# Kernel optimization log

Hardware: AMD Instinct MI355X
Metric: run time of the kernel (lower is better)

Reference implementation:

```python
import jax, jax.numpy as jnp
import numpy as np

INPUT_DIM = 1024
OUTPUT_DIM = 512
N_QUBITS = 12
DEPTH = 8
BATCH = 32768
LN_EPS = 1e-5
NOISE = 0.01


def setup_inputs() -> dict:
    key = jax.random.key(0)
    ks = jax.random.split(key, 12)
    inp = {
        "x": jax.random.normal(ks[0], (BATCH, INPUT_DIM), dtype=jnp.float32),
        "w_in": jax.random.normal(ks[1], (N_QUBITS, INPUT_DIM), dtype=jnp.float32) * 0.03,
        "b_in": jnp.zeros((N_QUBITS,), jnp.float32),
        "ln_g": jnp.ones((N_QUBITS,), jnp.float32),
        "ln_b": jnp.zeros((N_QUBITS,), jnp.float32),
        "rot": jax.random.normal(ks[2], (DEPTH, N_QUBITS, 3), dtype=jnp.float32) * 0.1,
        "ent": jax.random.normal(ks[3], (DEPTH, N_QUBITS - 1), dtype=jnp.float32) * 0.1,
        "w1": jax.random.normal(ks[4], (N_QUBITS, N_QUBITS), dtype=jnp.float32) * 0.3,
        "b1": jnp.zeros((N_QUBITS,), jnp.float32),
        "w2": jax.random.normal(ks[5], (OUTPUT_DIM, N_QUBITS), dtype=jnp.float32) * 0.3,
        "b2": jnp.zeros((OUTPUT_DIM,), jnp.float32),
        "meas_basis": jax.random.normal(ks[6], (N_QUBITS,), dtype=jnp.float32) * 0.1,
    }
    return inp


def _entangle(state, c):
    # c: sigmoid(ent[layer]) shape [n-1]. Effective (traced) torch semantics:
    # out[i]   = s[i]*(1-c_i)   + s[i+1]*c_i     for i in 0..n-2
    # out[n-1] = s[n-1]*(1-c_{n-2}) + s[n-2]*c_{n-2}
    left = state[:, :-1] * (1.0 - c) + state[:, 1:] * c          # [B, n-1]
    last = state[:, -1] * (1.0 - c[-1]) + state[:, -2] * c[-1]   # [B]
    return jnp.concatenate([left, last[:, None]], axis=1)


def reference(x, w_in, b_in, ln_g, ln_b, rot, ent, w1, b1, w2, b2, meas_basis):
    # input layer + layernorm + tanh
    h = x @ w_in.T + b_in                                   # [B, n]
    mu = jnp.mean(h, axis=-1, keepdims=True)
    var = jnp.mean((h - mu) ** 2, axis=-1, keepdims=True)
    h = (h - mu) * jax.lax.rsqrt(var + LN_EPS) * ln_g + ln_b
    h = jnp.tanh(h)

    encoded = h * jnp.float32(np.pi)
    state = jnp.zeros_like(encoded)
    for layer in range(DEPTH):
        rx = encoded + rot[layer, :, 0]
        state = state * jnp.cos(rx * 0.5) + jnp.sin(rot[layer, :, 1] * 0.5)
        state = state * jnp.cos(rot[layer, :, 2] * 0.5)     # Re(exp(i*rz/2))
        if layer < DEPTH - 1:
            state = _entangle(state, jax.nn.sigmoid(ent[layer]))

    # measurement: basis rotation + gaussian noise + tanh
    measured = state * jnp.tanh(meas_basis)
    noise = jax.random.normal(jax.random.key(1234), measured.shape, dtype=measured.dtype) * NOISE
    measured = jnp.tanh(measured + noise)

    # output MLP
    out = jax.nn.relu(measured @ w1.T + b1) @ w2.T + b2     # [B, OUTPUT_DIM]
    return out
```

## Files before the change

kernel.cpp:

```cpp
#include <hip/hip_runtime.h>
#include <cstdint>
#include <cstddef>


__device__ __forceinline__ uint32_t rotl32(uint32_t x, int r) {
  return (x << r) | (x >> (32 - r));
}

__device__ __forceinline__ void threefry2x32(uint32_t k0, uint32_t k1,
                                             uint32_t& x0, uint32_t& x1) {
  const uint32_t k2 = k0 ^ k1 ^ 0x1BD11BDAu;
  x0 += k0; x1 += k1;
#define TF_R(r) { x0 += x1; x1 = rotl32(x1, (r)); x1 ^= x0; }
  TF_R(13) TF_R(15) TF_R(26) TF_R(6)
  x0 += k1; x1 += k2 + 1u;
  TF_R(17) TF_R(29) TF_R(16) TF_R(24)
  x0 += k2; x1 += k0 + 2u;
  TF_R(13) TF_R(15) TF_R(26) TF_R(6)
  x0 += k0; x1 += k1 + 3u;
  TF_R(17) TF_R(29) TF_R(16) TF_R(24)
  x0 += k1; x1 += k2 + 4u;
  TF_R(13) TF_R(15) TF_R(26) TF_R(6)
  x0 += k2; x1 += k0 + 5u;
#undef TF_R
}

__device__ __forceinline__ float erfinv_xla(float x) {
  float w = -log1pf(-x * x);
  float p;
  if (w < 5.0f) {
    w -= 2.5f;
    p = 2.81022636e-08f;
    p = fmaf(p, w, 3.43273939e-07f);
    p = fmaf(p, w, -3.5233877e-06f);
    p = fmaf(p, w, -4.39150654e-06f);
    p = fmaf(p, w, 0.00021858087f);
    p = fmaf(p, w, -0.00125372503f);
    p = fmaf(p, w, -0.00417768164f);
    p = fmaf(p, w, 0.246640727f);
    p = fmaf(p, w, 1.50140941f);
  } else {
    w = sqrtf(w) - 3.0f;
    p = -0.000200214257f;
    p = fmaf(p, w, 0.000100950558f);
    p = fmaf(p, w, 0.00134934322f);
    p = fmaf(p, w, -0.00367342844f);
    p = fmaf(p, w, 0.00573950773f);
    p = fmaf(p, w, -0.0076224613f);
    p = fmaf(p, w, 0.00943887047f);
    p = fmaf(p, w, 1.00167406f);
    p = fmaf(p, w, 2.83297682f);
  }
  return p * x;
}

__global__ __launch_bounds__(512, 4)
void qnn_gemm_in(const float* __restrict__ x, const float* __restrict__ w_in,
                 const float* __restrict__ b_in, float* __restrict__ h) {
  __shared__ float wl[12 * 1024];
  {
    const float4* ws = (const float4*)w_in;
    float4* wd = (float4*)wl;
#pragma unroll
    for (int j = 0; j < 6; ++j) wd[threadIdx.x + 512 * j] = ws[threadIdx.x + 512 * j];
  }
  __syncthreads();

  const int wave = threadIdx.x >> 6;
  const int lane = threadIdx.x & 63;
  const int r    = lane >> 4;
  const int kc   = lane & 15;

  float bq[12];
#pragma unroll
  for (int q = 0; q < 12; ++q) bq[q] = b_in[q];

#pragma unroll
  for (int it = 0; it < 2; ++it) {
    const int row = (blockIdx.x << 6) + (wave << 3) + (it << 2) + r;
    const float4* xr = (const float4*)(x + (size_t)row * 1024);

    float4 A[4], B[4];
#pragma unroll
    for (int i = 0; i < 4; ++i) A[i] = xr[((0 + i) << 4) + kc];
#pragma unroll
    for (int i = 0; i < 4; ++i) B[i] = xr[((4 + i) << 4) + kc];

    float acc[12];
#pragma unroll
    for (int q = 0; q < 12; ++q) acc[q] = 0.0f;

#pragma unroll
    for (int i = 0; i < 4; ++i) {
      const int ks = i;
#pragma unroll
      for (int q = 0; q < 12; ++q) {
        const float4 wv = *(const float4*)&wl[q * 1024 + (ks << 6) + (kc << 2)];
        acc[q] += A[i].x * wv.x + A[i].y * wv.y + A[i].z * wv.z + A[i].w * wv.w;
      }
    }
#pragma unroll
    for (int i = 0; i < 4; ++i) A[i] = xr[((8 + i) << 4) + kc];

#pragma unroll
    for (int i = 0; i < 4; ++i) {
      const int ks = 4 + i;
#pragma unroll
      for (int q = 0; q < 12; ++q) {
        const float4 wv = *(const float4*)&wl[q * 1024 + (ks << 6) + (kc << 2)];
        acc[q] += B[i].x * wv.x + B[i].y * wv.y + B[i].z * wv.z + B[i].w * wv.w;
      }
    }
#pragma unroll
    for (int i = 0; i < 4; ++i) B[i] = xr[((12 + i) << 4) + kc];

#pragma unroll
    for (int i = 0; i < 4; ++i) {
      const int ks = 8 + i;
#pragma unroll
      for (int q = 0; q < 12; ++q) {
        const float4 wv = *(const float4*)&wl[q * 1024 + (ks << 6) + (kc << 2)];
        acc[q] += A[i].x * wv.x + A[i].y * wv.y + A[i].z * wv.z + A[i].w * wv.w;
      }
    }
#pragma unroll
    for (int i = 0; i < 4; ++i) {
      const int ks = 12 + i;
#pragma unroll
      for (int q = 0; q < 12; ++q) {
        const float4 wv = *(const float4*)&wl[q * 1024 + (ks << 6) + (kc << 2)];
        acc[q] += B[i].x * wv.x + B[i].y * wv.y + B[i].z * wv.z + B[i].w * wv.w;
      }
    }

#pragma unroll
    for (int q = 0; q < 12; ++q) {
      float v = acc[q];
      v += __shfl_xor(v, 1);
      v += __shfl_xor(v, 2);
      v += __shfl_xor(v, 4);
      v += __shfl_xor(v, 8);
      acc[q] = v + bq[q];
    }
    if (kc == 0) {
      float* hp = h + (size_t)row * 12;
      *(float4*)(hp + 0) = make_float4(acc[0], acc[1], acc[2], acc[3]);
      *(float4*)(hp + 4) = make_float4(acc[4], acc[5], acc[6], acc[7]);
      *(float4*)(hp + 8) = make_float4(acc[8], acc[9], acc[10], acc[11]);
    }
  }
}

__global__ __launch_bounds__(256, 4)
void qnn_tail(const float* __restrict__ h_in,
              const float* __restrict__ ln_g, const float* __restrict__ ln_b,
              const float* __restrict__ rot,  const float* __restrict__ ent,
              const float* __restrict__ w1,   const float* __restrict__ b1,
              const float* __restrict__ w2,   const float* __restrict__ b2,
              const float* __restrict__ meas, float* __restrict__ out) {
  __shared__ float w2s[512 * 12];
  __shared__ float b2s[512];
  __shared__ float hid[32 * 12];
  __shared__ float rot0s[8 * 16], sr1s[8 * 16], cr2s[8 * 16], cens[8 * 16];
  __shared__ float tmbs[16], w1T[12 * 16], b1s[16], lgs[16], lbs[16];

  const int t = threadIdx.x;

  {
    const float4* s = (const float4*)w2;
    float4* d = (float4*)w2s;
#pragma unroll
    for (int j = 0; j < 6; ++j) d[t + 256 * j] = s[t + 256 * j];
    if (t < 128) ((float4*)b2s)[t] = ((const float4*)b2)[t];
    if (t < 96) {
      const int l = t / 12, q = t % 12, base = (l * 12 + q) * 3;
      rot0s[l * 16 + q] = rot[base + 0];
      sr1s[l * 16 + q]  = sinf(rot[base + 1] * 0.5f);
      cr2s[l * 16 + q]  = cosf(rot[base + 2] * 0.5f);
    }
    if (t >= 96 && t < 184) {
      const int i = t - 96, l = i / 11, q = i % 11;
      cens[l * 16 + q] = 1.0f / (1.0f + expf(-ent[l * 11 + q]));
    }
    if (t >= 184 && t < 196) tmbs[t - 184] = tanhf(meas[t - 184]);
    if (t >= 196 && t < 208) b1s[t - 196] = b1[t - 196];
    if (t >= 208 && t < 220) lgs[t - 208] = ln_g[t - 208];
    if (t >= 220 && t < 232) lbs[t - 220] = ln_b[t - 220];
    if (t < 144) { const int j = t / 12, q = t % 12; w1T[q * 16 + j] = w1[t]; }
  }
  __syncthreads();

  float wa[12], wb[12];
#pragma unroll
  for (int q = 0; q < 12; ++q) {
    wa[q] = w2s[t * 12 + q];
    wb[q] = w2s[(t + 256) * 12 + q];
  }
  const float ba = b2s[t], bb = b2s[t + 256];

  const int lane = t & 63;
  const int wv   = t >> 6;
  const int grp  = lane >> 4;
  const int q    = lane & 15;
  const int gb   = lane & 48;
  const bool act = (q < 12);
  const int cidx = (q == 11) ? 10 : q;

#pragma unroll
  for (int pass = 0; pass < 2; ++pass) {
    const int rl  = (pass << 4) + (wv << 2) + grp;
    const int row = (blockIdx.x << 5) + rl;

    float hq = act ? h_in[(size_t)row * 12 + q] : 0.0f;

    float s = hq;
    s += __shfl_xor(s, 1); s += __shfl_xor(s, 2);
    s += __shfl_xor(s, 4); s += __shfl_xor(s, 8);
    const float mu = s * (1.0f / 12.0f);
    float d = act ? (hq - mu) : 0.0f;
    float v2 = d * d;
    v2 += __shfl_xor(v2, 1); v2 += __shfl_xor(v2, 2);
    v2 += __shfl_xor(v2, 4); v2 += __shfl_xor(v2, 8);
    const float inv = 1.0f / sqrtf(v2 * (1.0f / 12.0f) + 1e-5f);

    const float n   = d * inv * lgs[q] + lbs[q];
    const float enc = tanhf(n) * 3.14159265358979f;

    float st = 0.0f;
#pragma unroll
    for (int l = 0; l < 8; ++l) {
      const float rx = enc + rot0s[l * 16 + q];
      st = st * cosf(rx * 0.5f) + sr1s[l * 16 + q];
      st *= cr2s[l * 16 + q];
      if (l < 7) {
        const float stn = __shfl(st, lane + 1);
        const float stp = __shfl(st, lane - 1);
        const float c   = cens[l * 16 + cidx];
        const float other = (q == 11) ? stp : stn;
        st = st * (1.0f - c) + other * c;
      }
    }

    uint32_t x0 = 0u, x1 = (uint32_t)row * 12u + (uint32_t)q;
    threefry2x32(0u, 1234u, x0, x1);
    const uint32_t bits = x0 ^ x1;
    const float u01 = __uint_as_float((bits >> 9) | 0x3F800000u) - 1.0f;
    float u = u01 * 2.0f + (-0.99999994f);
    u = fmaxf(-0.99999994f, u);
    const float nrm = 1.41421356237f * erfinv_xla(u);
    const float m = tanhf(st * tmbs[q] + nrm * 0.01f);

    float acc1 = b1s[q];
#pragma unroll
    for (int qq = 0; qq < 12; ++qq) {
      const float mq = __shfl(m, gb + qq);
      acc1 = fmaf(mq, w1T[qq * 16 + q], acc1);
    }
    if (act) hid[rl * 12 + q] = fmaxf(acc1, 0.0f);
  }
  __syncthreads();

  float* ob = out + (size_t)blockIdx.x * 32 * 512;
  for (int rr = 0; rr < 32; ++rr) {
    const float4 h0 = *(const float4*)&hid[rr * 12 + 0];
    const float4 h1 = *(const float4*)&hid[rr * 12 + 4];
    const float4 h2 = *(const float4*)&hid[rr * 12 + 8];
    const float hvv[12] = {h0.x, h0.y, h0.z, h0.w, h1.x, h1.y, h1.z, h1.w,
                           h2.x, h2.y, h2.z, h2.w};
    float a = ba, b = bb;
#pragma unroll
    for (int qq = 0; qq < 12; ++qq) {
      a = fmaf(hvv[qq], wa[qq], a);
      b = fmaf(hvv[qq], wb[qq], b);
    }
    ob[rr * 512 + t] = a;
    ob[rr * 512 + 256 + t] = b;
  }
}

extern "C" void kernel_launch(void* const* d_in, const int* in_sizes, int n_in,
                              void* d_out, int out_size, void* d_ws, size_t ws_size,
                              hipStream_t stream) {
  const float* x    = (const float*)d_in[0];
  const float* w_in = (const float*)d_in[1];
  const float* b_in = (const float*)d_in[2];
  const float* ln_g = (const float*)d_in[3];
  const float* ln_b = (const float*)d_in[4];
  const float* rot  = (const float*)d_in[5];
  const float* ent  = (const float*)d_in[6];
  const float* w1   = (const float*)d_in[7];
  const float* b1   = (const float*)d_in[8];
  const float* w2   = (const float*)d_in[9];
  const float* b2   = (const float*)d_in[10];
  const float* mb   = (const float*)d_in[11];
  float* outp = (float*)d_out;
  float* h    = (float*)d_ws;

  qnn_gemm_in<<<512, 512, 0, stream>>>(x, w_in, b_in, h);
  qnn_tail<<<1024, 256, 0, stream>>>(h, ln_g, ln_b, rot, ent, w1, b1, w2, b2, mb, outp);
}
```

Baseline: 250.0 us.

## Restructure input GEMM so each wave processes four rows with shared weight loads

The input projection kernel now gives each wave four rows at once, with every lane covering a strided slice of K. Each LDS weight float4 is reused across four rows instead of one, and accumulation uses fused multiply-adds. Blocks shrink to 256 threads and the grid doubles to 1024. The trade-offs are a full 64-lane shuffle reduction per output, a larger register footprint (48 accumulators plus 16 float4 inputs), and a more serialized global load pattern per wave.

```diff
diff --git a/kernel.cpp b/kernel.cpp
--- a/kernel.cpp
+++ b/kernel.cpp
@@ -54,7 +54,7 @@
   return p * x;
 }
 
-__global__ __launch_bounds__(512, 4)
+__global__ __launch_bounds__(256, 2)
 void qnn_gemm_in(const float* __restrict__ x, const float* __restrict__ w_in,
                  const float* __restrict__ b_in, float* __restrict__ h) {
   __shared__ float wl[12 * 1024];
@@ -62,91 +62,65 @@
     const float4* ws = (const float4*)w_in;
     float4* wd = (float4*)wl;
 #pragma unroll
-    for (int j = 0; j < 6; ++j) wd[threadIdx.x + 512 * j] = ws[threadIdx.x + 512 * j];
+    for (int j = 0; j < 12; ++j) wd[threadIdx.x + 256 * j] = ws[threadIdx.x + 256 * j];
   }
   __syncthreads();
 
   const int wave = threadIdx.x >> 6;
   const int lane = threadIdx.x & 63;
-  const int r    = lane >> 4;
-  const int kc   = lane & 15;
-
-  float bq[12];
-#pragma unroll
-  for (int q = 0; q < 12; ++q) bq[q] = b_in[q];
-
-#pragma unroll
-  for (int it = 0; it < 2; ++it) {
-    const int row = (blockIdx.x << 6) + (wave << 3) + (it << 2) + r;
-    const float4* xr = (const float4*)(x + (size_t)row * 1024);
-
-    float4 A[4], B[4];
-#pragma unroll
-    for (int i = 0; i < 4; ++i) A[i] = xr[((0 + i) << 4) + kc];
-#pragma unroll
-    for (int i = 0; i < 4; ++i) B[i] = xr[((4 + i) << 4) + kc];
-
-    float acc[12];
-#pragma unroll
-    for (int q = 0; q < 12; ++q) acc[q] = 0.0f;
-
-#pragma unroll
-    for (int i = 0; i < 4; ++i) {
-      const int ks = i;
+  const float bmy = (lane < 12) ? b_in[lane] : 0.0f;
+
+#pragma unroll
+  for (int blk = 0; blk < 2; ++blk) {
+    const int row0 = (blockIdx.x << 5) + (wave << 3) + (blk << 2);
+
+    float4 xv[4][4];
+#pragma unroll
+    for (int r = 0; r < 4; ++r) {
+      const float4* xr = (const float4*)(x + (size_t)(row0 + r) * 1024);
+#pragma unroll
+      for (int ks = 0; ks < 4; ++ks) xv[r][ks] = xr[(ks << 6) + lane];
+    }
+
+    float acc[4][12];
+#pragma unroll
+    for (int r = 0; r < 4; ++r)
+#pragma unroll
+      for (int q = 0; q < 12; ++q) acc[r][q] = 0.0f;
+
+#pragma unroll
+    for (int q = 0; q < 12; ++q) {
+#pragma unroll
+      for (int ks = 0; ks < 4; ++ks) {
+        const float4 wv = *(const float4*)&wl[q * 1024 + (ks << 8) + (lane << 2)];
+#pragma unroll
+        for (int r = 0; r < 4; ++r) {
+          acc[r][q] = fmaf(xv[r][ks].x, wv.x,
+                      fmaf(xv[r][ks].y, wv.y,
+                      fmaf(xv[r][ks].z, wv.z,
+                      fmaf(xv[r][ks].w, wv.w, acc[r][q]))));
+        }
+      }
+    }
+
+#pragma unroll
+    for (int r = 0; r < 4; ++r) {
+      float hv[12];
 #pragma unroll
       for (int q = 0; q < 12; ++q) {
-        const float4 wv = *(const float4*)&wl[q * 1024 + (ks << 6) + (kc << 2)];
-        acc[q] += A[i].x * wv.x + A[i].y * wv.y + A[i].z * wv.z + A[i].w * wv.w;
+        float v = acc[r][q];
+        v += __shfl_xor(v, 1);
+        v += __shfl_xor(v, 2);
+        v += __shfl_xor(v, 4);
+        v += __shfl_xor(v, 8);
+        v += __shfl_xor(v, 16);
+        v += __shfl_xor(v, 32);
+        hv[q] = v;
       }
-    }
-#pragma unroll
-    for (int i = 0; i < 4; ++i) A[i] = xr[((8 + i) << 4) + kc];
-
-#pragma unroll
-    for (int i = 0; i < 4; ++i) {
-      const int ks = 4 + i;
-#pragma unroll
-      for (int q = 0; q < 12; ++q) {
-        const float4 wv = *(const float4*)&wl[q * 1024 + (ks << 6) + (kc << 2)];
-        acc[q] += B[i].x * wv.x + B[i].y * wv.y + B[i].z * wv.z + B[i].w * wv.w;
-      }
-    }
-#pragma unroll
-    for (int i = 0; i < 4; ++i) B[i] = xr[((12 + i) << 4) + kc];
-
-#pragma unroll
-    for (int i = 0; i < 4; ++i) {
-      const int ks = 8 + i;
-#pragma unroll
-      for (int q = 0; q < 12; ++q) {
-        const float4 wv = *(const float4*)&wl[q * 1024 + (ks << 6) + (kc << 2)];
-        acc[q] += A[i].x * wv.x + A[i].y * wv.y + A[i].z * wv.z + A[i].w * wv.w;
-      }
-    }
-#pragma unroll
-    for (int i = 0; i < 4; ++i) {
-      const int ks = 12 + i;
-#pragma unroll
-      for (int q = 0; q < 12; ++q) {
-        const float4 wv = *(const float4*)&wl[q * 1024 + (ks << 6) + (kc << 2)];
-        acc[q] += B[i].x * wv.x + B[i].y * wv.y + B[i].z * wv.z + B[i].w * wv.w;
-      }
-    }
-
-#pragma unroll
-    for (int q = 0; q < 12; ++q) {
-      float v = acc[q];
-      v += __shfl_xor(v, 1);
-      v += __shfl_xor(v, 2);
-      v += __shfl_xor(v, 4);
-      v += __shfl_xor(v, 8);
-      acc[q] = v + bq[q];
-    }
-    if (kc == 0) {
-      float* hp = h + (size_t)row * 12;
-      *(float4*)(hp + 0) = make_float4(acc[0], acc[1], acc[2], acc[3]);
-      *(float4*)(hp + 4) = make_float4(acc[4], acc[5], acc[6], acc[7]);
-      *(float4*)(hp + 8) = make_float4(acc[8], acc[9], acc[10], acc[11]);
+      float outv = hv[0];
+#pragma unroll
+      for (int q = 1; q < 12; ++q) outv = (lane == q) ? hv[q] : outv;
+      if (lane < 12) h[(size_t)(row0 + r) * 12 + lane] = outv + bmy;
     }
   }
 }
@@ -296,6 +270,6 @@
   float* outp = (float*)d_out;
   float* h    = (float*)d_ws;
 
-  qnn_gemm_in<<<512, 512, 0, stream>>>(x, w_in, b_in, h);
+  qnn_gemm_in<<<1024, 256, 0, stream>>>(x, w_in, b_in, h);
   qnn_tail<<<1024, 256, 0, stream>>>(h, ln_g, ln_b, rot, ent, w1, b1, w2, b2, mb, outp);
 }
```

New measurement: 272.5 us. 9.0% more time.

## Read input-projection weights directly from global memory and shrink GEMM blocks

Applied to the files above, without the earlier changes.

Stops staging the 48KB w_in matrix in shared memory and reads weight float4s straight from global memory, relying on L1/L2 caching. Blocks shrink to 256 threads handling 16 rows each, with a 2048-block grid instead of 512 blocks of 64 rows. This removes the per-block LDS fill and barrier, and lowers LDS use so more blocks can be resident. In exchange, every block fetches the weights again through cache, and the manual double-buffered prefetch of x is replaced by a plain unrolled loop.

```diff
diff --git a/kernel.cpp b/kernel.cpp
--- a/kernel.cpp
+++ b/kernel.cpp
@@ -54,100 +54,49 @@
   return p * x;
 }
 
-__global__ __launch_bounds__(512, 4)
+__global__ __launch_bounds__(256, 4)
 void qnn_gemm_in(const float* __restrict__ x, const float* __restrict__ w_in,
                  const float* __restrict__ b_in, float* __restrict__ h) {
-  __shared__ float wl[12 * 1024];
-  {
-    const float4* ws = (const float4*)w_in;
-    float4* wd = (float4*)wl;
-#pragma unroll
-    for (int j = 0; j < 6; ++j) wd[threadIdx.x + 512 * j] = ws[threadIdx.x + 512 * j];
-  }
-  __syncthreads();
-
   const int wave = threadIdx.x >> 6;
   const int lane = threadIdx.x & 63;
   const int r    = lane >> 4;
   const int kc   = lane & 15;
 
+  const int row = (blockIdx.x << 4) + (wave << 2) + r;
+  const float4* xr = (const float4*)(x + (size_t)row * 1024);
+
   float bq[12];
 #pragma unroll
   for (int q = 0; q < 12; ++q) bq[q] = b_in[q];
 
-#pragma unroll
-  for (int it = 0; it < 2; ++it) {
-    const int row = (blockIdx.x << 6) + (wave << 3) + (it << 2) + r;
-    const float4* xr = (const float4*)(x + (size_t)row * 1024);
-
-    float4 A[4], B[4];
-#pragma unroll
-    for (int i = 0; i < 4; ++i) A[i] = xr[((0 + i) << 4) + kc];
-#pragma unroll
-    for (int i = 0; i < 4; ++i) B[i] = xr[((4 + i) << 4) + kc];
-
-    float acc[12];
-#pragma unroll
-    for (int q = 0; q < 12; ++q) acc[q] = 0.0f;
-
-#pragma unroll
-    for (int i = 0; i < 4; ++i) {
-      const int ks = i;
-#pragma unroll
-      for (int q = 0; q < 12; ++q) {
-        const float4 wv = *(const float4*)&wl[q * 1024 + (ks << 6) + (kc << 2)];
-        acc[q] += A[i].x * wv.x + A[i].y * wv.y + A[i].z * wv.z + A[i].w * wv.w;
-      }
-    }
-#pragma unroll
-    for (int i = 0; i < 4; ++i) A[i] = xr[((8 + i) << 4) + kc];
-
-#pragma unroll
-    for (int i = 0; i < 4; ++i) {
-      const int ks = 4 + i;
-#pragma unroll
-      for (int q = 0; q < 12; ++q) {
-        const float4 wv = *(const float4*)&wl[q * 1024 + (ks << 6) + (kc << 2)];
-        acc[q] += B[i].x * wv.x + B[i].y * wv.y + B[i].z * wv.z + B[i].w * wv.w;
-      }
-    }
-#pragma unroll
-    for (int i = 0; i < 4; ++i) B[i] = xr[((12 + i) << 4) + kc];
-
-#pragma unroll
-    for (int i = 0; i < 4; ++i) {
-      const int ks = 8 + i;
-#pragma unroll
-      for (int q = 0; q < 12; ++q) {
-        const float4 wv = *(const float4*)&wl[q * 1024 + (ks << 6) + (kc << 2)];
-        acc[q] += A[i].x * wv.x + A[i].y * wv.y + A[i].z * wv.z + A[i].w * wv.w;
-      }
-    }
-#pragma unroll
-    for (int i = 0; i < 4; ++i) {
-      const int ks = 12 + i;
-#pragma unroll
-      for (int q = 0; q < 12; ++q) {
-        const float4 wv = *(const float4*)&wl[q * 1024 + (ks << 6) + (kc << 2)];
-        acc[q] += B[i].x * wv.x + B[i].y * wv.y + B[i].z * wv.z + B[i].w * wv.w;
-      }
-    }
-
+  float acc[12];
+#pragma unroll
+  for (int q = 0; q < 12; ++q) acc[q] = 0.0f;
+
+#pragma unroll 4
+  for (int ks = 0; ks < 16; ++ks) {
+    const float4 xv = xr[(ks << 4) + kc];
 #pragma unroll
     for (int q = 0; q < 12; ++q) {
-      float v = acc[q];
-      v += __shfl_xor(v, 1);
-      v += __shfl_xor(v, 2);
-      v += __shfl_xor(v, 4);
-      v += __shfl_xor(v, 8);
-      acc[q] = v + bq[q];
-    }
-    if (kc == 0) {
-      float* hp = h + (size_t)row * 12;
-      *(float4*)(hp + 0) = make_float4(acc[0], acc[1], acc[2], acc[3]);
-      *(float4*)(hp + 4) = make_float4(acc[4], acc[5], acc[6], acc[7]);
-      *(float4*)(hp + 8) = make_float4(acc[8], acc[9], acc[10], acc[11]);
-    }
+      const float4 wv = *(const float4*)&w_in[q * 1024 + (ks << 6) + (kc << 2)];
+      acc[q] += xv.x * wv.x + xv.y * wv.y + xv.z * wv.z + xv.w * wv.w;
+    }
+  }
+
+#pragma unroll
+  for (int q = 0; q < 12; ++q) {
+    float v = acc[q];
+    v += __shfl_xor(v, 1);
+    v += __shfl_xor(v, 2);
+    v += __shfl_xor(v, 4);
+    v += __shfl_xor(v, 8);
+    acc[q] = v + bq[q];
+  }
+  if (kc == 0) {
+    float* hp = h + (size_t)row * 12;
+    *(float4*)(hp + 0) = make_float4(acc[0], acc[1], acc[2], acc[3]);
+    *(float4*)(hp + 4) = make_float4(acc[4], acc[5], acc[6], acc[7]);
+    *(float4*)(hp + 8) = make_float4(acc[8], acc[9], acc[10], acc[11]);
   }
 }
 
@@ -296,6 +245,6 @@
   float* outp = (float*)d_out;
   float* h    = (float*)d_ws;
 
-  qnn_gemm_in<<<512, 512, 0, stream>>>(x, w_in, b_in, h);
+  qnn_gemm_in<<<2048, 256, 0, stream>>>(x, w_in, b_in, h);
   qnn_tail<<<1024, 256, 0, stream>>>(h, ln_g, ln_b, rot, ent, w1, b1, w2, b2, mb, outp);
 }
```

Result: slower. 284.2 us (+13.7%).
